# Kernel optimization log

Hardware: AMD Instinct MI355X
Metric: run time of the kernel (lower is better)

## Reference

```python
import jax, jax.numpy as jnp
import numpy as np

SHRINK_THRES = 0.0025
EPS = 1e-12  # F.normalize default eps


def _l2norm(v, axis=-1):
    return v / jnp.maximum(jnp.linalg.norm(v, axis=axis, keepdims=True), EPS)


def setup_inputs() -> dict:
    key = jax.random.key(0)
    ks = jax.random.split(key, 5)
    N, C, H, W = 16, 256, 64, 64
    mem_dim = 512
    x = jax.random.normal(ks[0], (N, C, H, W), dtype=jnp.float32)
    memory = jax.random.normal(ks[1], (mem_dim, C), dtype=jnp.float32) * 0.1
    memory = _l2norm(memory, axis=1)
    w1 = jax.random.normal(ks[2], (C, C // 2), dtype=jnp.float32) * (1.0 / np.sqrt(C))
    b1 = jnp.zeros((C // 2,), dtype=jnp.float32)
    w2 = jax.random.normal(ks[3], (C // 2, C), dtype=jnp.float32) * (1.0 / np.sqrt(C // 2))
    b2 = jnp.zeros((C,), dtype=jnp.float32)
    return {"x": x, "memory": memory, "w1": w1, "b1": b1, "w2": w2, "b2": b2}


def reference(x, memory, w1, b1, w2, b2):
    N, C, H, W = x.shape
    # [N,C,H,W] -> [N*H*W, C]
    x_flat = jnp.transpose(x, (0, 2, 3, 1)).reshape(-1, C)
    x_norm = _l2norm(x_flat, axis=1)
    # shared MLP over memory slots: Linear -> ReLU -> Linear -> ReLU
    m = jax.nn.relu(memory @ w1 + b1)
    m = jax.nn.relu(m @ w2 + b2)
    mem_norm = _l2norm(m, axis=1)  # [M, C]
    # cosine similarity + softmax over memory slots
    att = jax.nn.softmax(x_norm @ mem_norm.T, axis=1)  # [N*H*W, M]
    # hard shrink + L1 renormalization
    att = jax.nn.relu(att - SHRINK_THRES)
    att = att / jnp.maximum(jnp.sum(att, axis=1, keepdims=True), EPS)
    out_flat = att @ mem_norm  # [N*H*W, C]
    output = jnp.transpose(out_flat.reshape(N, H, W, C), (0, 3, 1, 2))
    att_map = jnp.transpose(att.reshape(N, H, W, -1), (0, 3, 1, 2))
    return output, att_map
```

## Files before the change

### kernel.cpp

```cpp
#include <hip/hip_runtime.h>
#include <hip/hip_bf16.h>

typedef _Float16 half8 __attribute__((ext_vector_type(8)));
typedef _Float16 half4v __attribute__((ext_vector_type(4)));
typedef float floatx4 __attribute__((ext_vector_type(4)));

#define C_DIM 256
#define M_DIM 512
#define HW 4096
#define TAU 0.0025f

__global__ __launch_bounds__(128) void prep_kernel(
    const float* __restrict__ memory, const float* __restrict__ w1,
    const float* __restrict__ b1, const float* __restrict__ w2,
    const float* __restrict__ b2,
    _Float16* __restrict__ mN, _Float16* __restrict__ mNt)
{
  __shared__ float sm[256];
  __shared__ float sh[128];
  __shared__ float s_part[2];
  __shared__ float s_tot;
  const int r = blockIdx.x;
  const int t = threadIdx.x;
  sm[t]       = memory[r * C_DIM + t];
  sm[t + 128] = memory[r * C_DIM + t + 128];
  __syncthreads();
  float acc = b1[t];
#pragma unroll 8
  for (int c = 0; c < 256; ++c) acc = fmaf(sm[c], w1[c * 128 + t], acc);
  sh[t] = fmaxf(acc, 0.f);
  __syncthreads();
  float o0 = b2[t], o1 = b2[t + 128];
#pragma unroll 8
  for (int k = 0; k < 128; ++k) {
    float h = sh[k];
    o0 = fmaf(h, w2[k * 256 + t], o0);
    o1 = fmaf(h, w2[k * 256 + t + 128], o1);
  }
  o0 = fmaxf(o0, 0.f);
  o1 = fmaxf(o1, 0.f);
  float ss = o0 * o0 + o1 * o1;
#pragma unroll
  for (int off = 32; off >= 1; off >>= 1) ss += __shfl_down(ss, off);
  if ((t & 63) == 0) s_part[t >> 6] = ss;
  __syncthreads();
  if (t == 0) s_tot = s_part[0] + s_part[1];
  __syncthreads();
  const float inv = 1.f / fmaxf(sqrtf(s_tot), 1e-12f);
  const float v0 = o0 * inv, v1 = o1 * inv;
  const _Float16 h0 = (_Float16)v0, h1 = (_Float16)v1;
  mN[r * C_DIM + t]         = h0;
  mN[r * C_DIM + t + 128]   = h1;
  mNt[t * M_DIM + r]        = h0;
  mNt[(t + 128) * M_DIM + r] = h1;
}

__global__ __launch_bounds__(512, 6) void main_kernel(
    const float* __restrict__ x,
    const _Float16* __restrict__ mN,
    const _Float16* __restrict__ mNt,
    float* __restrict__ out, float* __restrict__ attmap)
{
  __shared__ __align__(16) unsigned char smem_u[33280];
  __shared__ float s_red[32][8];
  __shared__ float s_stat[32];
  __shared__ float s_sumsq[32];

  _Float16 (*Xh)[264]   = (_Float16(*)[264])smem_u;
  _Float16 (*attb)[520] = (_Float16(*)[520])smem_u;
  float    (*Ost)[260]  = (float(*)[260])smem_u;

  const int tid  = threadIdx.x;
  const int wave = tid >> 6;
  const int lane = tid & 63;
  const int q    = lane >> 4;
  const int c16  = lane & 15;
  const int px   = tid & 31;
  const int cg   = tid >> 5;

  const int blk = blockIdx.x;
  const int img = blk >> 7;
  const int hw0 = (blk & 127) * 32;
  const float* __restrict__ xb = x + (size_t)img * C_DIM * HW + hw0;

  if (tid < 32) s_sumsq[tid] = 0.f;
  __syncthreads();

  float part = 0.f;
#pragma unroll
  for (int i = 0; i < 4; ++i) {
    const int cb = i * 64 + cg * 4;
    const float v0 = xb[(size_t)(cb + 0) * HW + px];
    const float v1 = xb[(size_t)(cb + 1) * HW + px];
    const float v2 = xb[(size_t)(cb + 2) * HW + px];
    const float v3 = xb[(size_t)(cb + 3) * HW + px];
    part += v0 * v0 + v1 * v1 + v2 * v2 + v3 * v3;
    half4v hv = {(_Float16)v0, (_Float16)v1, (_Float16)v2, (_Float16)v3};
    *(half4v*)&Xh[px][cb] = hv;
  }
  atomicAdd(&s_sumsq[px], part);
  __syncthreads();

  floatx4 acc[2][4];
#pragma unroll
  for (int mt = 0; mt < 2; ++mt)
#pragma unroll
    for (int nt = 0; nt < 4; ++nt) {
      floatx4 z = {0.f, 0.f, 0.f, 0.f};
      acc[mt][nt] = z;
    }

#pragma unroll
  for (int kb = 0; kb < 8; ++kb) {
    const int k0 = kb * 32 + q * 8;
    half8 ah[2];
#pragma unroll
    for (int mt = 0; mt < 2; ++mt) ah[mt] = *(const half8*)&Xh[mt * 16 + c16][k0];
#pragma unroll
    for (int nt = 0; nt < 4; ++nt) {
      const int n = wave * 64 + nt * 16 + c16;
      const half8 bh = *(const half8*)(mN + (size_t)n * C_DIM + k0);
#pragma unroll
      for (int mt = 0; mt < 2; ++mt)
        acc[mt][nt] = __builtin_amdgcn_mfma_f32_16x16x32_f16(ah[mt], bh, acc[mt][nt], 0, 0, 0);
    }
  }

#pragma unroll
  for (int mt = 0; mt < 2; ++mt)
#pragma unroll
    for (int r = 0; r < 4; ++r) {
      const int m = mt * 16 + q * 4 + r;
      const float iv = 1.f / fmaxf(sqrtf(s_sumsq[m]), 1e-12f);
      float s = 0.f;
#pragma unroll
      for (int nt = 0; nt < 4; ++nt) {
        const float e = __expf(acc[mt][nt][r] * iv);
        acc[mt][nt][r] = e;
        s += e;
      }
      s += __shfl_xor(s, 1);
      s += __shfl_xor(s, 2);
      s += __shfl_xor(s, 4);
      s += __shfl_xor(s, 8);
      if (c16 == 0) s_red[m][wave] = s;
    }
  __syncthreads();
  if (tid < 32) {
    float v = 0.f;
#pragma unroll
    for (int w = 0; w < 8; ++w) v += s_red[tid][w];
    s_stat[tid] = 1.f / v;
  }
  __syncthreads();

#pragma unroll
  for (int mt = 0; mt < 2; ++mt)
#pragma unroll
    for (int r = 0; r < 4; ++r) {
      const int m = mt * 16 + q * 4 + r;
      const float isum = s_stat[m];
      float s = 0.f;
#pragma unroll
      for (int nt = 0; nt < 4; ++nt) {
        const float tv = fmaxf(acc[mt][nt][r] * isum - TAU, 0.f);
        acc[mt][nt][r] = tv;
        s += tv;
      }
      s += __shfl_xor(s, 1);
      s += __shfl_xor(s, 2);
      s += __shfl_xor(s, 4);
      s += __shfl_xor(s, 8);
      if (c16 == 0) s_red[m][wave] = s;
    }
  __syncthreads();
  if (tid < 32) {
    float v = 0.f;
#pragma unroll
    for (int w = 0; w < 8; ++w) v += s_red[tid][w];
    s_stat[tid] = 1.f / fmaxf(v, 1e-12f);
  }
  __syncthreads();

#pragma unroll
  for (int mt = 0; mt < 2; ++mt)
#pragma unroll
    for (int r = 0; r < 4; ++r) {
      const int m = mt * 16 + q * 4 + r;
      const float rs = s_stat[m];
#pragma unroll
      for (int nt = 0; nt < 4; ++nt)
        attb[m][wave * 64 + nt * 16 + c16] = (_Float16)(acc[mt][nt][r] * rs);
    }
  __syncthreads();

#pragma unroll
  for (int i = 0; i < 8; ++i) {
    const int n0 = (cg + 16 * i) * 4;
    const half4v v = *(const half4v*)&attb[px][n0];
    float* dst = attmap + ((size_t)img * M_DIM + n0) * HW + hw0 + px;
    dst[0]            = (float)v[0];
    dst[(size_t)HW]   = (float)v[1];
    dst[(size_t)2*HW] = (float)v[2];
    dst[(size_t)3*HW] = (float)v[3];
  }

  floatx4 acc2[2][2];
#pragma unroll
  for (int mt = 0; mt < 2; ++mt)
#pragma unroll
    for (int ct = 0; ct < 2; ++ct) {
      floatx4 z = {0.f, 0.f, 0.f, 0.f};
      acc2[mt][ct] = z;
    }
#pragma unroll
  for (int kb = 0; kb < 16; ++kb) {
    const int k0 = kb * 32 + q * 8;
    half8 a[2];
#pragma unroll
    for (int mt = 0; mt < 2; ++mt) a[mt] = *(const half8*)&attb[mt * 16 + c16][k0];
#pragma unroll
    for (int ct = 0; ct < 2; ++ct) {
      const int cc = wave * 32 + ct * 16 + c16;
      const half8 b = *(const half8*)(mNt + (size_t)cc * M_DIM + k0);
#pragma unroll
      for (int mt = 0; mt < 2; ++mt)
        acc2[mt][ct] = __builtin_amdgcn_mfma_f32_16x16x32_f16(a[mt], b, acc2[mt][ct], 0, 0, 0);
    }
  }
  __syncthreads();

#pragma unroll
  for (int mt = 0; mt < 2; ++mt)
#pragma unroll
    for (int ct = 0; ct < 2; ++ct)
#pragma unroll
      for (int r = 0; r < 4; ++r)
        Ost[mt * 16 + q * 4 + r][wave * 32 + ct * 16 + c16] = acc2[mt][ct][r];
  __syncthreads();
#pragma unroll
  for (int i = 0; i < 4; ++i) {
    const int c0 = (cg + 16 * i) * 4;
    const floatx4 v = *(const floatx4*)&Ost[px][c0];
    float* dst = out + ((size_t)img * C_DIM + c0) * HW + hw0 + px;
    dst[0]            = v[0];
    dst[(size_t)HW]   = v[1];
    dst[(size_t)2*HW] = v[2];
    dst[(size_t)3*HW] = v[3];
  }
}

extern "C" void kernel_launch(void* const* d_in, const int* in_sizes, int n_in,
                              void* d_out, int out_size, void* d_ws, size_t ws_size,
                              hipStream_t stream) {
  (void)in_sizes; (void)n_in; (void)out_size; (void)ws_size;
  const float* x      = (const float*)d_in[0];
  const float* memory = (const float*)d_in[1];
  const float* w1     = (const float*)d_in[2];
  const float* b1     = (const float*)d_in[3];
  const float* w2     = (const float*)d_in[4];
  const float* b2     = (const float*)d_in[5];
  float* out    = (float*)d_out;
  float* attmap = out + (size_t)16 * C_DIM * HW;

  _Float16* mN  = (_Float16*)d_ws;
  _Float16* mNt = mN + (size_t)M_DIM * C_DIM;

  hipLaunchKernelGGL(prep_kernel, dim3(M_DIM), dim3(128), 0, stream,
                     memory, w1, b1, w2, b2, mN, mNt);
  hipLaunchKernelGGL(main_kernel, dim3(2048), dim3(512), 0, stream,
                     x, mN, mNt, out, attmap);
}
```

Measured before the change: 399.0 us.

## Vectorize x loads, prefetch B fragments, and use atomic softmax row sums

The x tile is now read as float4 vectors across 4 pixels per thread, with sum-of-squares reduced by shuffles before the shared atomics. Both MFMA loops software-prefetch the next k-step's global B fragments into registers. The two cross-wave reductions switch from a shared table plus single-thread finalize to shared atomics, which removes two barriers. Launch bounds drop the occupancy hint from 6 to 4 blocks to leave room for the extra prefetch registers, at the cost of fewer resident waves.

```diff
diff --git a/kernel.cpp b/kernel.cpp
--- a/kernel.cpp
+++ b/kernel.cpp
@@ -55,16 +55,18 @@
   mNt[(t + 128) * M_DIM + r] = h1;
 }
 
-__global__ __launch_bounds__(512, 6) void main_kernel(
+#define MFMA16(a, b, c) __builtin_amdgcn_mfma_f32_16x16x32_f16(a, b, c, 0, 0, 0)
+
+__global__ __launch_bounds__(512, 4) void main_kernel(
     const float* __restrict__ x,
     const _Float16* __restrict__ mN,
     const _Float16* __restrict__ mNt,
     float* __restrict__ out, float* __restrict__ attmap)
 {
   __shared__ __align__(16) unsigned char smem_u[33280];
-  __shared__ float s_red[32][8];
-  __shared__ float s_stat[32];
   __shared__ float s_sumsq[32];
+  __shared__ float s_sum1[32];
+  __shared__ float s_sum2[32];
 
   _Float16 (*Xh)[264]   = (_Float16(*)[264])smem_u;
   _Float16 (*attb)[520] = (_Float16(*)[520])smem_u;
@@ -77,28 +79,39 @@
   const int c16  = lane & 15;
   const int px   = tid & 31;
   const int cg   = tid >> 5;
+  const int g    = tid >> 3;
+  const int pxq  = tid & 7;
 
   const int blk = blockIdx.x;
   const int img = blk >> 7;
   const int hw0 = (blk & 127) * 32;
   const float* __restrict__ xb = x + (size_t)img * C_DIM * HW + hw0;
 
-  if (tid < 32) s_sumsq[tid] = 0.f;
-  __syncthreads();
-
-  float part = 0.f;
-#pragma unroll
-  for (int i = 0; i < 4; ++i) {
-    const int cb = i * 64 + cg * 4;
-    const float v0 = xb[(size_t)(cb + 0) * HW + px];
-    const float v1 = xb[(size_t)(cb + 1) * HW + px];
-    const float v2 = xb[(size_t)(cb + 2) * HW + px];
-    const float v3 = xb[(size_t)(cb + 3) * HW + px];
-    part += v0 * v0 + v1 * v1 + v2 * v2 + v3 * v3;
-    half4v hv = {(_Float16)v0, (_Float16)v1, (_Float16)v2, (_Float16)v3};
-    *(half4v*)&Xh[px][cb] = hv;
-  }
-  atomicAdd(&s_sumsq[px], part);
+  if (tid < 32) { s_sumsq[tid] = 0.f; s_sum1[tid] = 0.f; s_sum2[tid] = 0.f; }
+  __syncthreads();
+
+  {
+    floatx4 v[4];
+#pragma unroll
+    for (int i = 0; i < 4; ++i)
+      v[i] = *(const floatx4*)(xb + (size_t)(4 * g + i) * HW + pxq * 4);
+    float ps[4];
+#pragma unroll
+    for (int j = 0; j < 4; ++j) {
+      const int p = pxq * 4 + j;
+      half4v hv = {(_Float16)v[0][j], (_Float16)v[1][j], (_Float16)v[2][j], (_Float16)v[3][j]};
+      *(half4v*)&Xh[p][4 * g] = hv;
+      ps[j] = v[0][j] * v[0][j] + v[1][j] * v[1][j] + v[2][j] * v[2][j] + v[3][j] * v[3][j];
+    }
+#pragma unroll
+    for (int off = 8; off < 64; off <<= 1)
+#pragma unroll
+      for (int j = 0; j < 4; ++j) ps[j] += __shfl_xor(ps[j], off);
+    if ((lane >> 3) == 0) {
+#pragma unroll
+      for (int j = 0; j < 4; ++j) atomicAdd(&s_sumsq[(lane & 7) * 4 + j], ps[j]);
+    }
+  }
   __syncthreads();
 
   floatx4 acc[2][4];
@@ -109,20 +122,30 @@
       floatx4 z = {0.f, 0.f, 0.f, 0.f};
       acc[mt][nt] = z;
     }
-
-#pragma unroll
-  for (int kb = 0; kb < 8; ++kb) {
-    const int k0 = kb * 32 + q * 8;
-    half8 ah[2];
-#pragma unroll
-    for (int mt = 0; mt < 2; ++mt) ah[mt] = *(const half8*)&Xh[mt * 16 + c16][k0];
-#pragma unroll
-    for (int nt = 0; nt < 4; ++nt) {
-      const int n = wave * 64 + nt * 16 + c16;
-      const half8 bh = *(const half8*)(mN + (size_t)n * C_DIM + k0);
-#pragma unroll
-      for (int mt = 0; mt < 2; ++mt)
-        acc[mt][nt] = __builtin_amdgcn_mfma_f32_16x16x32_f16(ah[mt], bh, acc[mt][nt], 0, 0, 0);
+  {
+    const _Float16* bp[4];
+#pragma unroll
+    for (int nt = 0; nt < 4; ++nt)
+      bp[nt] = mN + (size_t)(wave * 64 + nt * 16 + c16) * C_DIM + q * 8;
+    half8 bcur[4], bnxt[4];
+#pragma unroll
+    for (int nt = 0; nt < 4; ++nt) bcur[nt] = *(const half8*)bp[nt];
+#pragma unroll
+    for (int kb = 0; kb < 8; ++kb) {
+      if (kb < 7) {
+#pragma unroll
+        for (int nt = 0; nt < 4; ++nt) bnxt[nt] = *(const half8*)(bp[nt] + (kb + 1) * 32);
+      }
+      const int k0 = kb * 32 + q * 8;
+      const half8 ah0 = *(const half8*)&Xh[c16][k0];
+      const half8 ah1 = *(const half8*)&Xh[16 + c16][k0];
+#pragma unroll
+      for (int nt = 0; nt < 4; ++nt) {
+        acc[0][nt] = MFMA16(ah0, bcur[nt], acc[0][nt]);
+        acc[1][nt] = MFMA16(ah1, bcur[nt], acc[1][nt]);
+      }
+#pragma unroll
+      for (int nt = 0; nt < 4; ++nt) bcur[nt] = bnxt[nt];
     }
   }
 
@@ -143,15 +166,8 @@
       s += __shfl_xor(s, 2);
       s += __shfl_xor(s, 4);
       s += __shfl_xor(s, 8);
-      if (c16 == 0) s_red[m][wave] = s;
-    }
-  __syncthreads();
-  if (tid < 32) {
-    float v = 0.f;
-#pragma unroll
-    for (int w = 0; w < 8; ++w) v += s_red[tid][w];
-    s_stat[tid] = 1.f / v;
-  }
+      if (c16 == 0) atomicAdd(&s_sum1[m], s);
+    }
   __syncthreads();
 
 #pragma unroll
@@ -159,7 +175,7 @@
 #pragma unroll
     for (int r = 0; r < 4; ++r) {
       const int m = mt * 16 + q * 4 + r;
-      const float isum = s_stat[m];
+      const float isum = 1.f / s_sum1[m];
       float s = 0.f;
 #pragma unroll
       for (int nt = 0; nt < 4; ++nt) {
@@ -171,15 +187,8 @@
       s += __shfl_xor(s, 2);
       s += __shfl_xor(s, 4);
       s += __shfl_xor(s, 8);
-      if (c16 == 0) s_red[m][wave] = s;
-    }
-  __syncthreads();
-  if (tid < 32) {
-    float v = 0.f;
-#pragma unroll
-    for (int w = 0; w < 8; ++w) v += s_red[tid][w];
-    s_stat[tid] = 1.f / fmaxf(v, 1e-12f);
-  }
+      if (c16 == 0) atomicAdd(&s_sum2[m], s);
+    }
   __syncthreads();
 
 #pragma unroll
@@ -187,7 +196,7 @@
 #pragma unroll
     for (int r = 0; r < 4; ++r) {
       const int m = mt * 16 + q * 4 + r;
-      const float rs = s_stat[m];
+      const float rs = 1.f / fmaxf(s_sum2[m], 1e-12f);
 #pragma unroll
       for (int nt = 0; nt < 4; ++nt)
         attb[m][wave * 64 + nt * 16 + c16] = (_Float16)(acc[mt][nt][r] * rs);
@@ -213,19 +222,30 @@
       floatx4 z = {0.f, 0.f, 0.f, 0.f};
       acc2[mt][ct] = z;
     }
-#pragma unroll
-  for (int kb = 0; kb < 16; ++kb) {
-    const int k0 = kb * 32 + q * 8;
-    half8 a[2];
-#pragma unroll
-    for (int mt = 0; mt < 2; ++mt) a[mt] = *(const half8*)&attb[mt * 16 + c16][k0];
-#pragma unroll
-    for (int ct = 0; ct < 2; ++ct) {
-      const int cc = wave * 32 + ct * 16 + c16;
-      const half8 b = *(const half8*)(mNt + (size_t)cc * M_DIM + k0);
-#pragma unroll
-      for (int mt = 0; mt < 2; ++mt)
-        acc2[mt][ct] = __builtin_amdgcn_mfma_f32_16x16x32_f16(a[mt], b, acc2[mt][ct], 0, 0, 0);
+  {
+    const _Float16* bp2[2];
+#pragma unroll
+    for (int ct = 0; ct < 2; ++ct)
+      bp2[ct] = mNt + (size_t)(wave * 32 + ct * 16 + c16) * M_DIM + q * 8;
+    half8 bcur[2], bnxt[2];
+#pragma unroll
+    for (int ct = 0; ct < 2; ++ct) bcur[ct] = *(const half8*)bp2[ct];
+#pragma unroll
+    for (int kb = 0; kb < 16; ++kb) {
+      if (kb < 15) {
+#pragma unroll
+        for (int ct = 0; ct < 2; ++ct) bnxt[ct] = *(const half8*)(bp2[ct] + (kb + 1) * 32);
+      }
+      const int k0 = kb * 32 + q * 8;
+      const half8 a0 = *(const half8*)&attb[c16][k0];
+      const half8 a1 = *(const half8*)&attb[16 + c16][k0];
+#pragma unroll
+      for (int ct = 0; ct < 2; ++ct) {
+        acc2[0][ct] = MFMA16(a0, bcur[ct], acc2[0][ct]);
+        acc2[1][ct] = MFMA16(a1, bcur[ct], acc2[1][ct]);
+      }
+#pragma unroll
+      for (int ct = 0; ct < 2; ++ct) bcur[ct] = bnxt[ct];
     }
   }
   __syncthreads();
```

Measured after the change: 380.7 us. 1.05x faster.
